# Optimization experiments

Hardware: AMD Instinct MI355X
Metric: run time of the kernel (lower is better)

Reference implementation:

```python
import jax, jax.numpy as jnp
import numpy as np

N, E, D, L, G = 10000, 320000, 256, 5, 128
RWSE, DEG_V = 16, 1001
BN_EPS = 1e-5


def setup_inputs() -> dict:
    key = jax.random.key(0)
    ks = jax.random.split(key, 12)
    s = 1.0 / np.sqrt(D)
    return {
        'feat_id': jax.random.randint(ks[0], (N,), 0, 100000, dtype=jnp.int64 if jax.config.jax_enable_x64 else jnp.int32),
        'edge_index': jax.random.randint(ks[1], (2, E), 0, N),
        'batch_idx': jnp.sort(jax.random.randint(ks[2], (N,), 0, G)),
        'rwse': jax.random.normal(ks[3], (N, RWSE), jnp.float32),
        'in_degrees': jax.random.randint(ks[4], (N,), 0, DEG_V),
        # value_projection: Linear(fixed_input_dim=D -> D); stored as [in, out]
        'w_val': jax.random.normal(ks[5], (D, D), jnp.float32) * s,
        'b_val': jnp.zeros((D,), jnp.float32),
        # rwse_projection: Linear(RWSE -> D)
        'w_rwse': jax.random.normal(ks[6], (RWSE, D), jnp.float32) * (1.0 / np.sqrt(RWSE)),
        'b_rwse': jnp.zeros((D,), jnp.float32),
        # degree_embedding table (clamped to [0, 1000])
        'deg_emb': jax.random.normal(ks[7], (DEG_V, D), jnp.float32) * 0.02,
        # per-layer GIN MLP: Linear-ReLU-Linear, stacked over L layers
        'mlp_w1': jax.random.normal(ks[8], (L, D, D), jnp.float32) * s,
        'mlp_b1': jnp.zeros((L, D), jnp.float32),
        'mlp_w2': jax.random.normal(ks[9], (L, D, D), jnp.float32) * s,
        'mlp_b2': jnp.zeros((L, D), jnp.float32),
        # BatchNorm1d (eval mode: running stats)
        'bn_gamma': jnp.ones((L, D), jnp.float32),
        'bn_beta': jnp.zeros((L, D), jnp.float32),
        'bn_mean': jnp.zeros((L, D), jnp.float32),
        'bn_var': jax.random.uniform(ks[10], (L, D), jnp.float32, 0.5, 1.5),
        # GIN eps per layer
        'eps_gin': jnp.zeros((L,), jnp.float32),
    }


def reference(feat_id, edge_index, batch_idx, rwse, in_degrees,
              w_val, b_val, w_rwse, b_rwse, deg_emb,
              mlp_w1, mlp_b1, mlp_w2, mlp_b2,
              bn_gamma, bn_beta, bn_mean, bn_var, eps_gin):
    # --- node feature embedding ---
    h_id = jnp.remainder(feat_id, D)
    h_one = jax.nn.one_hot(h_id, D, dtype=jnp.float32)            # [N, D]
    h = h_one @ w_val + b_val + rwse @ w_rwse + b_rwse            # value + rwse projections
    deg = jnp.clip(in_degrees, 0, 1000)
    h = h + deg_emb[deg]                                          # degree embedding

    src, dst = edge_index[0], edge_index[1]
    for l in range(L):
        # GIN message passing: sum neighbor features into dst (gather -> scatter-add)
        agg = jax.ops.segment_sum(h[src], dst, num_segments=N)    # [N, D]
        y = agg + (1.0 + eps_gin[l]) * h
        # MLP (Linear-ReLU-Linear)
        y = jax.nn.relu(y @ mlp_w1[l] + mlp_b1[l]) @ mlp_w2[l] + mlp_b2[l]
        # BatchNorm1d (eval: running stats) + ReLU
        y = (y - bn_mean[l]) * (bn_gamma[l] * jax.lax.rsqrt(bn_var[l] + BN_EPS)) + bn_beta[l]
        h = jax.nn.relu(y)

    # --- mean pooling per graph ---
    sums = jax.ops.segment_sum(h, batch_idx, num_segments=G)                     # [G, D]
    cnt = jax.ops.segment_sum(jnp.ones((N, 1), h.dtype), batch_idx, num_segments=G)
    graph_feature = sums / jnp.maximum(cnt, 1.0)
    return graph_feature, h
```

## Files before the change

kernel.cpp:

```cpp
#include <hip/hip_runtime.h>
#include <hip/hip_bf16.h>

#define N_NODES 10000
#define N_EDGES 320000
#define DIM     256
#define N_LAYERS 5
#define N_GRAPHS 128
#define RWSE_K  16
#define GBM 16

typedef __bf16 bf16_t;
typedef bf16_t bf16x8 __attribute__((ext_vector_type(8)));
typedef float  f32x4  __attribute__((ext_vector_type(4)));

__device__ inline ushort f2bf(float f) {
    union { float f; unsigned u; } v; v.f = f;
    unsigned r = v.u + 0x7fff + ((v.u >> 16) & 1);
    return (ushort)(r >> 16);
}
__device__ inline float bfbits2f(unsigned hi16) {
    union { unsigned u; float f; } v; v.u = hi16;
    return v.f;
}

__global__ __launch_bounds__(256)
void setup_kernel(const int* __restrict__ feat_id,
                  const float* __restrict__ rwse,
                  const int* __restrict__ in_deg,
                  const float* __restrict__ w_val,
                  const float* __restrict__ b_val,
                  const float* __restrict__ w_rwse,
                  const float* __restrict__ b_rwse,
                  const float* __restrict__ deg_emb,
                  ushort* __restrict__ hb,
                  const int* __restrict__ ei, int* __restrict__ cnt_arr,
                  const float* __restrict__ w1, const float* __restrict__ w2,
                  ushort* __restrict__ wt1, ushort* __restrict__ wt2,
                  const float* __restrict__ gamma, const float* __restrict__ beta,
                  const float* __restrict__ mean, const float* __restrict__ var,
                  const float* __restrict__ b2, float* __restrict__ scale,
                  float* __restrict__ shift) {
    __shared__ float r[RWSE_K];
    __shared__ float t[32][33];
    int b = blockIdx.x;
    int tid = threadIdx.x;
    if (b < N_NODES) {
        int i = b, d = tid;
        if (d < RWSE_K) r[d] = rwse[i * RWSE_K + d];
        __syncthreads();
        int hid = feat_id[i] & (DIM - 1);
        int dg = in_deg[i];
        dg = dg < 0 ? 0 : (dg > 1000 ? 1000 : dg);
        float v = w_val[hid * DIM + d] + b_val[d] + b_rwse[d] + deg_emb[dg * DIM + d];
#pragma unroll
        for (int k = 0; k < RWSE_K; ++k) v += r[k] * w_rwse[k * DIM + d];
        hb[i * DIM + d] = f2bf(v);
    } else if (b < 11250) {
        int e = (b - N_NODES) * 256 + tid;
        if (e < N_EDGES) atomicAdd(&cnt_arr[ei[N_EDGES + e]], 1);
    } else if (b < 11890) {
        int w_id = b - 11250;
        int l = w_id >> 7;
        int rem = w_id & 127;
        int mat = rem >> 6;
        int tile = rem & 63;
        const float* W  = (mat ? w2  : w1)  + (size_t)l * DIM * DIM;
        ushort*      Wt = (mat ? wt2 : wt1) + (size_t)l * DIM * DIM;
        int k0 = (tile >> 3) * 32, n0 = (tile & 7) * 32;
        int tx = tid & 31, ty = tid >> 5;
#pragma unroll
        for (int j = 0; j < 4; ++j)
            t[ty + j * 8][tx] = W[(k0 + ty + j * 8) * DIM + n0 + tx];
        __syncthreads();
#pragma unroll
        for (int j = 0; j < 4; ++j)
            Wt[(n0 + ty + j * 8) * DIM + k0 + tx] = f2bf(t[tx][ty + j * 8]);
    } else {
        int l = b - 11890;
        int idx = l * DIM + tid;
        float s = gamma[idx] * rsqrtf(var[idx] + 1e-5f);
        scale[idx] = s;
        shift[idx] = beta[idx] + (b2[idx] - mean[idx]) * s;
    }
}

__global__ __launch_bounds__(1024)
void scan_kernel(const int* __restrict__ cnt_arr, int* __restrict__ cur, int n) {
    __shared__ int wsum[16];
    __shared__ int carry_sh;
    int tid = threadIdx.x, wave = tid >> 6, lane = tid & 63;
    if (tid == 0) carry_sh = 0;
    __syncthreads();
    for (int base = 0; base < n; base += 1024) {
        int idx = base + tid;
        int v = (idx < n) ? cnt_arr[idx] : 0;
        int s = v;
#pragma unroll
        for (int off = 1; off < 64; off <<= 1) {
            int t = __shfl_up(s, off, 64);
            if (lane >= off) s += t;
        }
        if (lane == 63) wsum[wave] = s;
        __syncthreads();
        if (wave == 0) {
            int ws = (lane < 16) ? wsum[lane] : 0;
#pragma unroll
            for (int off = 1; off < 16; off <<= 1) {
                int t = __shfl_up(ws, off, 64);
                if (lane >= off) ws += t;
            }
            if (lane < 16) wsum[lane] = ws;
        }
        __syncthreads();
        int excl = s - v + (wave ? wsum[wave - 1] : 0) + carry_sh;
        if (idx < n) cur[idx] = excl;
        __syncthreads();
        if (tid == 0) carry_sh += wsum[15];
        __syncthreads();
    }
}

__global__ __launch_bounds__(256)
void fill_kernel(const int* __restrict__ ei, int* __restrict__ cur,
                 int* __restrict__ cs) {
    int e = blockIdx.x * 256 + threadIdx.x;
    if (e < N_EDGES) {
        int d = ei[N_EDGES + e];
        int p = atomicAdd(&cur[d], 1);
        cs[p] = ei[e];
    }
}

#define ACCV(v)                                                        \
    acc[0] += bfbits2f((v).x << 16); acc[1] += bfbits2f((v).x & 0xffff0000u); \
    acc[2] += bfbits2f((v).y << 16); acc[3] += bfbits2f((v).y & 0xffff0000u); \
    acc[4] += bfbits2f((v).z << 16); acc[5] += bfbits2f((v).z & 0xffff0000u); \
    acc[6] += bfbits2f((v).w << 16); acc[7] += bfbits2f((v).w & 0xffff0000u);

__global__ __launch_bounds__(256)
void agg_kernel(const ushort* __restrict__ hb,
                const int* __restrict__ cur, const int* __restrict__ cs,
                const float* __restrict__ eps_gin, int layer,
                ushort* __restrict__ y) {
    int wave = threadIdx.x >> 6;
    int lane = threadIdx.x & 63;
    int half = lane >> 5;
    int sl   = lane & 31;
    int i = blockIdx.x * 4 + wave;
    if (i >= N_NODES) return;
    const uint4* hb4 = (const uint4*)hb;
    float acc[8];
#pragma unroll
    for (int t = 0; t < 8; ++t) acc[t] = 0.f;

    int e0 = i ? cur[i - 1] : 0;
    int e1 = cur[i];
    for (int base = e0; base < e1; base += 64) {
        int rem = e1 - base;
        int cnt = rem < 64 ? rem : 64;
        int idx = (base + lane < e1) ? cs[base + lane] : 0;
        int j = 0;
        for (; j + 8 <= cnt; j += 8) {
            int s0 = __shfl(idx, j + half, 64);
            int s1 = __shfl(idx, j + 2 + half, 64);
            int s2 = __shfl(idx, j + 4 + half, 64);
            int s3 = __shfl(idx, j + 6 + half, 64);
            uint4 v0 = hb4[(size_t)s0 * 32 + sl];
            uint4 v1 = hb4[(size_t)s1 * 32 + sl];
            uint4 v2 = hb4[(size_t)s2 * 32 + sl];
            uint4 v3 = hb4[(size_t)s3 * 32 + sl];
            ACCV(v0); ACCV(v1); ACCV(v2); ACCV(v3);
        }
        for (; j + 2 <= cnt; j += 2) {
            int s = __shfl(idx, j + half, 64);
            uint4 v = hb4[(size_t)s * 32 + sl];
            ACCV(v);
        }
        if (j < cnt) {
            int s = __shfl(idx, j, 64);
            if (half == 0) {
                uint4 v = hb4[(size_t)s * 32 + sl];
                ACCV(v);
            }
        }
    }
#pragma unroll
    for (int t = 0; t < 8; ++t) acc[t] += __shfl_xor(acc[t], 32, 64);
    if (half == 0) {
        float sc = 1.0f + eps_gin[layer];
        uint4 sv = hb4[(size_t)i * 32 + sl];
        acc[0] += bfbits2f(sv.x << 16) * sc; acc[1] += bfbits2f(sv.x & 0xffff0000u) * sc;
        acc[2] += bfbits2f(sv.y << 16) * sc; acc[3] += bfbits2f(sv.y & 0xffff0000u) * sc;
        acc[4] += bfbits2f(sv.z << 16) * sc; acc[5] += bfbits2f(sv.z & 0xffff0000u) * sc;
        acc[6] += bfbits2f(sv.w << 16) * sc; acc[7] += bfbits2f(sv.w & 0xffff0000u) * sc;
        uint4 o;
        o.x = (uint)f2bf(acc[0]) | ((uint)f2bf(acc[1]) << 16);
        o.y = (uint)f2bf(acc[2]) | ((uint)f2bf(acc[3]) << 16);
        o.z = (uint)f2bf(acc[4]) | ((uint)f2bf(acc[5]) << 16);
        o.w = (uint)f2bf(acc[6]) | ((uint)f2bf(acc[7]) << 16);
        ((uint4*)y)[(size_t)i * 32 + sl] = o;
    }
}

__global__ __launch_bounds__(256)
void gemm12_kernel(const ushort* __restrict__ A, const ushort* __restrict__ Wt1,
                   const float* __restrict__ b1, const ushort* __restrict__ Wt2,
                   const float* __restrict__ bnsc, const float* __restrict__ bnsh,
                   float* __restrict__ outF, ushort* __restrict__ outB, int nrows) {
    __shared__ __align__(16) ushort As[GBM][40];
    __shared__ __align__(16) ushort Bs[DIM][40];
    __shared__ __align__(16) ushort Ts[GBM][DIM + 8];
    int tx = threadIdx.x;
    int row0 = blockIdx.x * GBM;
    int wave = tx >> 6, lane = tx & 63, quad = lane >> 4, l16 = lane & 15;
    int wc = wave * 64;
    int srow = tx >> 2;
    int skol = (tx & 3) * 8;

    f32x4 acc[4];
#pragma unroll
    for (int t = 0; t < 4; ++t) acc[t] = (f32x4){0.f, 0.f, 0.f, 0.f};

    for (int k0 = 0; k0 < DIM; k0 += 32) {
        if (tx < 64) {
            int arow = row0 + srow;
            uint4 av = make_uint4(0u, 0u, 0u, 0u);
            if (arow < nrows) av = *(const uint4*)&A[(size_t)arow * DIM + k0 + skol];
            *(uint4*)&As[srow][skol] = av;
        }
#pragma unroll
        for (int j = 0; j < 4; ++j) {
            int r = srow + 64 * j;
            *(uint4*)&Bs[r][skol] = *(const uint4*)&Wt1[(size_t)r * DIM + k0 + skol];
        }
        __syncthreads();
        bf16x8 af = *(const bf16x8*)&As[l16][quad * 8];
#pragma unroll
        for (int tj = 0; tj < 4; ++tj) {
            bf16x8 bf = *(const bf16x8*)&Bs[wc + tj * 16 + l16][quad * 8];
            acc[tj] = __builtin_amdgcn_mfma_f32_16x16x32_bf16(af, bf, acc[tj], 0, 0, 0);
        }
        __syncthreads();
    }
#pragma unroll
    for (int tj = 0; tj < 4; ++tj) {
        int col = wc + tj * 16 + l16;
        float bias = b1[col];
#pragma unroll
        for (int r = 0; r < 4; ++r)
            Ts[quad * 4 + r][col] = f2bf(fmaxf(acc[tj][r] + bias, 0.f));
    }
    __syncthreads();

#pragma unroll
    for (int t = 0; t < 4; ++t) acc[t] = (f32x4){0.f, 0.f, 0.f, 0.f};
    for (int k0 = 0; k0 < DIM; k0 += 32) {
#pragma unroll
        for (int j = 0; j < 4; ++j) {
            int r = srow + 64 * j;
            *(uint4*)&Bs[r][skol] = *(const uint4*)&Wt2[(size_t)r * DIM + k0 + skol];
        }
        __syncthreads();
        bf16x8 af = *(const bf16x8*)&Ts[l16][k0 + quad * 8];
#pragma unroll
        for (int tj = 0; tj < 4; ++tj) {
            bf16x8 bf = *(const bf16x8*)&Bs[wc + tj * 16 + l16][quad * 8];
            acc[tj] = __builtin_amdgcn_mfma_f32_16x16x32_bf16(af, bf, acc[tj], 0, 0, 0);
        }
        __syncthreads();
    }
#pragma unroll
    for (int tj = 0; tj < 4; ++tj) {
        int col = wc + tj * 16 + l16;
        float s = bnsc[col], sh = bnsh[col];
#pragma unroll
        for (int r = 0; r < 4; ++r) {
            int row = row0 + quad * 4 + r;
            if (row < nrows) {
                float v = fmaxf(acc[tj][r] * s + sh, 0.f);
                if (outF) outF[(size_t)row * DIM + col] = v;
                if (outB) outB[(size_t)row * DIM + col] = f2bf(v);
            }
        }
    }
}

__global__ __launch_bounds__(256)
void pool_kernel(const float* __restrict__ hfin, const int* __restrict__ batch,
                 float* __restrict__ out) {
    int g = blockIdx.x;
    int d = threadIdx.x;
    int l = 0, r = N_NODES;
    while (l < r) { int m = (l + r) >> 1; if (batch[m] < g) l = m + 1; else r = m; }
    int lo = l;
    r = N_NODES;
    while (l < r) { int m = (l + r) >> 1; if (batch[m] < g + 1) l = m + 1; else r = m; }
    int hi = l;
    float a0 = 0.f, a1 = 0.f, a2 = 0.f, a3 = 0.f;
    int i = lo;
    for (; i + 4 <= hi; i += 4) {
        a0 += hfin[(size_t)i * DIM + d];
        a1 += hfin[(size_t)(i + 1) * DIM + d];
        a2 += hfin[(size_t)(i + 2) * DIM + d];
        a3 += hfin[(size_t)(i + 3) * DIM + d];
    }
    for (; i < hi; ++i) a0 += hfin[(size_t)i * DIM + d];
    float c = (float)(hi - lo);
    if (c < 1.f) c = 1.f;
    out[g * DIM + d] = ((a0 + a1) + (a2 + a3)) / c;
}

extern "C" void kernel_launch(void* const* d_in, const int* in_sizes, int n_in,
                              void* d_out, int out_size, void* d_ws, size_t ws_size,
                              hipStream_t stream) {
    const int*   feat_id  = (const int*)d_in[0];
    const int*   ei       = (const int*)d_in[1];
    const int*   batch    = (const int*)d_in[2];
    const float* rwse     = (const float*)d_in[3];
    const int*   in_deg   = (const int*)d_in[4];
    const float* w_val    = (const float*)d_in[5];
    const float* b_val    = (const float*)d_in[6];
    const float* w_rwse   = (const float*)d_in[7];
    const float* b_rwse   = (const float*)d_in[8];
    const float* deg_emb  = (const float*)d_in[9];
    const float* mlp_w1   = (const float*)d_in[10];
    const float* mlp_b1   = (const float*)d_in[11];
    const float* mlp_w2   = (const float*)d_in[12];
    const float* mlp_b2   = (const float*)d_in[13];
    const float* bn_gamma = (const float*)d_in[14];
    const float* bn_beta  = (const float*)d_in[15];
    const float* bn_mean  = (const float*)d_in[16];
    const float* bn_var   = (const float*)d_in[17];
    const float* eps_gin  = (const float*)d_in[18];

    float* out = (float*)d_out;
    float* out_h = out + N_GRAPHS * DIM;

    char* w = (char*)d_ws;
    ushort* hb   = (ushort*)w;
    ushort* y    = hb + (size_t)N_NODES * DIM;
    ushort* wt1  = y + (size_t)N_NODES * DIM;
    ushort* wt2  = wt1 + (size_t)N_LAYERS * DIM * DIM;
    int* cnt_arr = (int*)(wt2 + (size_t)N_LAYERS * DIM * DIM);
    int* cur     = cnt_arr + N_NODES;
    int* cs      = cur + N_NODES;
    float* bnsc  = (float*)(cs + N_EDGES);
    float* bnsh  = bnsc + N_LAYERS * DIM;

    hipMemsetAsync(cnt_arr, 0, N_NODES * sizeof(int), stream);

    setup_kernel<<<11895, 256, 0, stream>>>(
        feat_id, rwse, in_deg, w_val, b_val, w_rwse, b_rwse, deg_emb,
        hb, ei, cnt_arr, mlp_w1, mlp_w2, wt1, wt2,
        bn_gamma, bn_beta, bn_mean, bn_var, mlp_b2, bnsc, bnsh);
    scan_kernel<<<1, 1024, 0, stream>>>(cnt_arr, cur, N_NODES);
    fill_kernel<<<(N_EDGES + 255) / 256, 256, 0, stream>>>(ei, cur, cs);

    int agrid = (N_NODES + 3) / 4;
    int ggrid = (N_NODES + GBM - 1) / GBM;
    for (int l = 0; l < N_LAYERS; ++l) {
        agg_kernel<<<agrid, 256, 0, stream>>>(hb, cur, cs, eps_gin, l, y);
        bool last = (l == N_LAYERS - 1);
        gemm12_kernel<<<ggrid, 256, 0, stream>>>(
            y, wt1 + (size_t)l * DIM * DIM, mlp_b1 + l * DIM,
            wt2 + (size_t)l * DIM * DIM, bnsc + l * DIM, bnsh + l * DIM,
            last ? out_h : nullptr, last ? nullptr : hb, N_NODES);
    }

    pool_kernel<<<N_GRAPHS, 256, 0, stream>>>(out_h, batch, out);
}
```

Before: 342.7 us.

## Load weight fragments directly from global memory in fused MLP GEMM, dropping LDS staging

The fused two-layer MLP kernel no longer stages weight tiles through shared memory each k-step. MFMA B-fragments are now read straight from global (L2-cached) weight arrays, and the whole 16-row A tile is loaded into LDS once, then reused as the intermediate buffer. This removes per-iteration barriers and LDS store/load traffic, and the k-loops are partially unrolled so more loads can be in flight. The cost is that every block re-reads both weight matrices from L2 with less-coalesced 16-byte accesses per lane, so performance depends on cache bandwidth and latency hiding.

After: 389.7 us. 1.14x slower.

```diff
diff --git a/kernel.cpp b/kernel.cpp
--- a/kernel.cpp
+++ b/kernel.cpp
@@ -207,68 +207,64 @@
                    const float* __restrict__ b1, const ushort* __restrict__ Wt2,
                    const float* __restrict__ bnsc, const float* __restrict__ bnsh,
                    float* __restrict__ outF, ushort* __restrict__ outB, int nrows) {
-    __shared__ __align__(16) ushort As[GBM][40];
-    __shared__ __align__(16) ushort Bs[DIM][40];
-    __shared__ __align__(16) ushort Ts[GBM][DIM + 8];
+    __shared__ __align__(16) ushort AT[GBM][DIM + 8];
     int tx = threadIdx.x;
     int row0 = blockIdx.x * GBM;
     int wave = tx >> 6, lane = tx & 63, quad = lane >> 4, l16 = lane & 15;
     int wc = wave * 64;
-    int srow = tx >> 2;
-    int skol = (tx & 3) * 8;
+
+    {
+        int r = tx >> 4;
+        int c = (tx & 15) * 16;
+        int arow = row0 + r;
+        uint4 av0 = make_uint4(0u, 0u, 0u, 0u);
+        uint4 av1 = make_uint4(0u, 0u, 0u, 0u);
+        if (arow < nrows) {
+            av0 = *(const uint4*)&A[(size_t)arow * DIM + c];
+            av1 = *(const uint4*)&A[(size_t)arow * DIM + c + 8];
+        }
+        *(uint4*)&AT[r][c] = av0;
+        *(uint4*)&AT[r][c + 8] = av1;
+    }
+    __syncthreads();
 
     f32x4 acc[4];
 #pragma unroll
     for (int t = 0; t < 4; ++t) acc[t] = (f32x4){0.f, 0.f, 0.f, 0.f};
 
+#pragma unroll 4
     for (int k0 = 0; k0 < DIM; k0 += 32) {
-        if (tx < 64) {
-            int arow = row0 + srow;
-            uint4 av = make_uint4(0u, 0u, 0u, 0u);
-            if (arow < nrows) av = *(const uint4*)&A[(size_t)arow * DIM + k0 + skol];
-            *(uint4*)&As[srow][skol] = av;
-        }
-#pragma unroll
-        for (int j = 0; j < 4; ++j) {
-            int r = srow + 64 * j;
-            *(uint4*)&Bs[r][skol] = *(const uint4*)&Wt1[(size_t)r * DIM + k0 + skol];
-        }
-        __syncthreads();
-        bf16x8 af = *(const bf16x8*)&As[l16][quad * 8];
+        bf16x8 af = *(const bf16x8*)&AT[l16][k0 + quad * 8];
 #pragma unroll
         for (int tj = 0; tj < 4; ++tj) {
-            bf16x8 bf = *(const bf16x8*)&Bs[wc + tj * 16 + l16][quad * 8];
+            bf16x8 bf = *(const bf16x8*)&Wt1[(size_t)(wc + tj * 16 + l16) * DIM + k0 + quad * 8];
             acc[tj] = __builtin_amdgcn_mfma_f32_16x16x32_bf16(af, bf, acc[tj], 0, 0, 0);
         }
-        __syncthreads();
-    }
+    }
+    __syncthreads();
+
 #pragma unroll
     for (int tj = 0; tj < 4; ++tj) {
         int col = wc + tj * 16 + l16;
         float bias = b1[col];
 #pragma unroll
         for (int r = 0; r < 4; ++r)
-            Ts[quad * 4 + r][col] = f2bf(fmaxf(acc[tj][r] + bias, 0.f));
+            AT[quad * 4 + r][col] = f2bf(fmaxf(acc[tj][r] + bias, 0.f));
     }
     __syncthreads();
 
 #pragma unroll
     for (int t = 0; t < 4; ++t) acc[t] = (f32x4){0.f, 0.f, 0.f, 0.f};
+#pragma unroll 4
     for (int k0 = 0; k0 < DIM; k0 += 32) {
-#pragma unroll
-        for (int j = 0; j < 4; ++j) {
-            int r = srow + 64 * j;
-            *(uint4*)&Bs[r][skol] = *(const uint4*)&Wt2[(size_t)r * DIM + k0 + skol];
-        }
-        __syncthreads();
-        bf16x8 af = *(const bf16x8*)&Ts[l16][k0 + quad * 8];
+        bf16x8 af = *(const bf16x8*)&AT[l16][k0 + quad * 8];
 #pragma unroll
         for (int tj = 0; tj < 4; ++tj) {
-            bf16x8 bf = *(const bf16x8*)&Bs[wc + tj * 16 + l16][quad * 8];
+            bf16x8 bf = *(const bf16x8*)&Wt2[(size_t)(wc + tj * 16 + l16) * DIM + k0 + quad * 8];
             acc[tj] = __builtin_amdgcn_mfma_f32_16x16x32_bf16(af, bf, acc[tj], 0, 0, 0);
         }
-        __syncthreads();
-    }
+    }
+
 #pragma unroll
     for (int tj = 0; tj < 4; ++tj) {
         int col = wc + tj * 16 + l16;
```

## Fuse per-layer aggregation, MLP and pooling into one cooperative persistent kernel

Applied to the files above, without the earlier changes.

Replaces the ten per-layer aggregation and GEMM launches plus the pooling launch with a single cooperative kernel. It loops over layers with grid-stride work and uses grid-wide barriers between the aggregation and MLP phases. The goal is to remove kernel launch overhead and inter-kernel gaps. The cost is that grid.sync barriers and a capped, occupancy-bounded grid size may leave load imbalance. A fallback to the original multi-kernel path is kept for when the cooperative launch fails.

Measured after the change: 1.202 ms. 3.51x slower.

```diff
diff --git a/kernel.cpp b/kernel.cpp
--- a/kernel.cpp
+++ b/kernel.cpp
@@ -1,5 +1,8 @@
 #include <hip/hip_runtime.h>
 #include <hip/hip_bf16.h>
+#include <hip/hip_cooperative_groups.h>
+
+namespace cg = cooperative_groups;
 
 #define N_NODES 10000
 #define N_EDGES 320000
@@ -8,6 +11,7 @@
 #define N_GRAPHS 128
 #define RWSE_K  16
 #define GBM 16
+#define NCHUNKS ((N_NODES + GBM - 1) / GBM)
 
 typedef __bf16 bf16_t;
 typedef bf16_t bf16x8 __attribute__((ext_vector_type(8)));
@@ -137,22 +141,14 @@
     acc[4] += bfbits2f((v).z << 16); acc[5] += bfbits2f((v).z & 0xffff0000u); \
     acc[6] += bfbits2f((v).w << 16); acc[7] += bfbits2f((v).w & 0xffff0000u);
 
-__global__ __launch_bounds__(256)
-void agg_kernel(const ushort* __restrict__ hb,
-                const int* __restrict__ cur, const int* __restrict__ cs,
-                const float* __restrict__ eps_gin, int layer,
-                ushort* __restrict__ y) {
-    int wave = threadIdx.x >> 6;
-    int lane = threadIdx.x & 63;
-    int half = lane >> 5;
-    int sl   = lane & 31;
-    int i = blockIdx.x * 4 + wave;
-    if (i >= N_NODES) return;
-    const uint4* hb4 = (const uint4*)hb;
+__device__ __forceinline__ void agg_node(int i, int lane, int half, int sl,
+                                         const uint4* hb4,
+                                         const int* __restrict__ cur,
+                                         const int* __restrict__ cs,
+                                         float sc, ushort* __restrict__ y) {
     float acc[8];
 #pragma unroll
     for (int t = 0; t < 8; ++t) acc[t] = 0.f;
-
     int e0 = i ? cur[i - 1] : 0;
     int e1 = cur[i];
     for (int base = e0; base < e1; base += 64) {
@@ -187,7 +183,6 @@
 #pragma unroll
     for (int t = 0; t < 8; ++t) acc[t] += __shfl_xor(acc[t], 32, 64);
     if (half == 0) {
-        float sc = 1.0f + eps_gin[layer];
         uint4 sv = hb4[(size_t)i * 32 + sl];
         acc[0] += bfbits2f(sv.x << 16) * sc; acc[1] += bfbits2f(sv.x & 0xffff0000u) * sc;
         acc[2] += bfbits2f(sv.y << 16) * sc; acc[3] += bfbits2f(sv.y & 0xffff0000u) * sc;
@@ -202,30 +197,21 @@
     }
 }
 
-__global__ __launch_bounds__(256)
-void gemm12_kernel(const ushort* __restrict__ A, const ushort* __restrict__ Wt1,
-                   const float* __restrict__ b1, const ushort* __restrict__ Wt2,
-                   const float* __restrict__ bnsc, const float* __restrict__ bnsh,
-                   float* __restrict__ outF, ushort* __restrict__ outB, int nrows) {
-    __shared__ __align__(16) ushort As[GBM][40];
-    __shared__ __align__(16) ushort Bs[DIM][40];
-    __shared__ __align__(16) ushort Ts[GBM][DIM + 8];
-    int tx = threadIdx.x;
-    int row0 = blockIdx.x * GBM;
-    int wave = tx >> 6, lane = tx & 63, quad = lane >> 4, l16 = lane & 15;
-    int wc = wave * 64;
-    int srow = tx >> 2;
-    int skol = (tx & 3) * 8;
-
+__device__ __forceinline__ void mlp_chunk(
+        int row0, int tx, int wave, int quad, int l16, int srow, int skol, int wc,
+        ushort (*As)[40], ushort (*Bs)[40], ushort (*Ts)[DIM + 8],
+        const ushort* __restrict__ Ain, const ushort* __restrict__ Wt1,
+        const float* __restrict__ b1, const ushort* __restrict__ Wt2,
+        const float* __restrict__ bnsc, const float* __restrict__ bnsh,
+        float* __restrict__ outF, ushort* __restrict__ outB) {
     f32x4 acc[4];
 #pragma unroll
     for (int t = 0; t < 4; ++t) acc[t] = (f32x4){0.f, 0.f, 0.f, 0.f};
-
     for (int k0 = 0; k0 < DIM; k0 += 32) {
         if (tx < 64) {
             int arow = row0 + srow;
             uint4 av = make_uint4(0u, 0u, 0u, 0u);
-            if (arow < nrows) av = *(const uint4*)&A[(size_t)arow * DIM + k0 + skol];
+            if (arow < N_NODES) av = *(const uint4*)&Ain[(size_t)arow * DIM + k0 + skol];
             *(uint4*)&As[srow][skol] = av;
         }
 #pragma unroll
@@ -251,7 +237,6 @@
             Ts[quad * 4 + r][col] = f2bf(fmaxf(acc[tj][r] + bias, 0.f));
     }
     __syncthreads();
-
 #pragma unroll
     for (int t = 0; t < 4; ++t) acc[t] = (f32x4){0.f, 0.f, 0.f, 0.f};
     for (int k0 = 0; k0 < DIM; k0 += 32) {
@@ -276,7 +261,7 @@
 #pragma unroll
         for (int r = 0; r < 4; ++r) {
             int row = row0 + quad * 4 + r;
-            if (row < nrows) {
+            if (row < N_NODES) {
                 float v = fmaxf(acc[tj][r] * s + sh, 0.f);
                 if (outF) outF[(size_t)row * DIM + col] = v;
                 if (outB) outB[(size_t)row * DIM + col] = f2bf(v);
@@ -285,11 +270,9 @@
     }
 }
 
-__global__ __launch_bounds__(256)
-void pool_kernel(const float* __restrict__ hfin, const int* __restrict__ batch,
-                 float* __restrict__ out) {
-    int g = blockIdx.x;
-    int d = threadIdx.x;
+__device__ __forceinline__ void pool_graph(int g, int d, const float* __restrict__ out_h,
+                                           const int* __restrict__ batch,
+                                           float* __restrict__ out) {
     int l = 0, r = N_NODES;
     while (l < r) { int m = (l + r) >> 1; if (batch[m] < g) l = m + 1; else r = m; }
     int lo = l;
@@ -299,15 +282,93 @@
     float a0 = 0.f, a1 = 0.f, a2 = 0.f, a3 = 0.f;
     int i = lo;
     for (; i + 4 <= hi; i += 4) {
-        a0 += hfin[(size_t)i * DIM + d];
-        a1 += hfin[(size_t)(i + 1) * DIM + d];
-        a2 += hfin[(size_t)(i + 2) * DIM + d];
-        a3 += hfin[(size_t)(i + 3) * DIM + d];
-    }
-    for (; i < hi; ++i) a0 += hfin[(size_t)i * DIM + d];
+        a0 += out_h[(size_t)i * DIM + d];
+        a1 += out_h[(size_t)(i + 1) * DIM + d];
+        a2 += out_h[(size_t)(i + 2) * DIM + d];
+        a3 += out_h[(size_t)(i + 3) * DIM + d];
+    }
+    for (; i < hi; ++i) a0 += out_h[(size_t)i * DIM + d];
     float c = (float)(hi - lo);
     if (c < 1.f) c = 1.f;
     out[g * DIM + d] = ((a0 + a1) + (a2 + a3)) / c;
+}
+
+__global__ __launch_bounds__(256, 4)
+void net_kernel(ushort* __restrict__ hb, ushort* __restrict__ y,
+                const int* __restrict__ cur, const int* __restrict__ cs,
+                const float* __restrict__ eps_gin,
+                const ushort* __restrict__ wt1, const ushort* __restrict__ wt2,
+                const float* __restrict__ b1all,
+                const float* __restrict__ bnscAll, const float* __restrict__ bnshAll,
+                const int* __restrict__ batch, float* __restrict__ out) {
+    cg::grid_group grid = cg::this_grid();
+    __shared__ __align__(16) ushort As[GBM][40];
+    __shared__ __align__(16) ushort Bs[DIM][40];
+    __shared__ __align__(16) ushort Ts[GBM][DIM + 8];
+    float* out_h = out + N_GRAPHS * DIM;
+
+    int tx = threadIdx.x;
+    int wave = tx >> 6, lane = tx & 63, half = lane >> 5, sl = lane & 31;
+    int quad = lane >> 4, l16 = lane & 15;
+    int gwave = blockIdx.x * 4 + wave;
+    const int nwaves = gridDim.x * 4;
+    int srow = tx >> 2;
+    int skol = (tx & 3) * 8;
+    int wc = wave * 64;
+
+    for (int l = 0; l < N_LAYERS; ++l) {
+        float sc = 1.0f + eps_gin[l];
+        const uint4* hb4 = (const uint4*)hb;
+        for (int i = gwave; i < N_NODES; i += nwaves)
+            agg_node(i, lane, half, sl, hb4, cur, cs, sc, y);
+        grid.sync();
+
+        const ushort* Wt1 = wt1 + (size_t)l * DIM * DIM;
+        const ushort* Wt2 = wt2 + (size_t)l * DIM * DIM;
+        bool last = (l == N_LAYERS - 1);
+        for (int c = blockIdx.x; c < NCHUNKS; c += gridDim.x)
+            mlp_chunk(c * GBM, tx, wave, quad, l16, srow, skol, wc, As, Bs, Ts,
+                      y, Wt1, b1all + l * DIM, Wt2,
+                      bnscAll + l * DIM, bnshAll + l * DIM,
+                      last ? out_h : nullptr, last ? nullptr : hb);
+        grid.sync();
+    }
+
+    if (blockIdx.x < N_GRAPHS)
+        pool_graph(blockIdx.x, tx, out_h, batch, out);
+}
+
+__global__ __launch_bounds__(256)
+void agg_kernel(const ushort* __restrict__ hb,
+                const int* __restrict__ cur, const int* __restrict__ cs,
+                const float* __restrict__ eps_gin, int layer,
+                ushort* __restrict__ y) {
+    int wave = threadIdx.x >> 6;
+    int lane = threadIdx.x & 63;
+    int i = blockIdx.x * 4 + wave;
+    if (i >= N_NODES) return;
+    agg_node(i, lane, lane >> 5, lane & 31, (const uint4*)hb, cur, cs,
+             1.0f + eps_gin[layer], y);
+}
+
+__global__ __launch_bounds__(256)
+void gemm12_kernel(const ushort* __restrict__ A, const ushort* __restrict__ Wt1,
+                   const float* __restrict__ b1, const ushort* __restrict__ Wt2,
+                   const float* __restrict__ bnsc, const float* __restrict__ bnsh,
+                   float* __restrict__ outF, ushort* __restrict__ outB) {
+    __shared__ __align__(16) ushort As[GBM][40];
+    __shared__ __align__(16) ushort Bs[DIM][40];
+    __shared__ __align__(16) ushort Ts[GBM][DIM + 8];
+    int tx = threadIdx.x;
+    int wave = tx >> 6, lane = tx & 63, quad = lane >> 4, l16 = lane & 15;
+    mlp_chunk(blockIdx.x * GBM, tx, wave, quad, l16, tx >> 2, (tx & 3) * 8,
+              wave * 64, As, Bs, Ts, A, Wt1, b1, Wt2, bnsc, bnsh, outF, outB);
+}
+
+__global__ __launch_bounds__(256)
+void pool_kernel(const float* __restrict__ hfin, const int* __restrict__ batch,
+                 float* __restrict__ out) {
+    pool_graph(blockIdx.x, threadIdx.x, hfin, batch, out);
 }
 
 extern "C" void kernel_launch(void* const* d_in, const int* in_sizes, int n_in,
@@ -356,16 +417,35 @@
     scan_kernel<<<1, 1024, 0, stream>>>(cnt_arr, cur, N_NODES);
     fill_kernel<<<(N_EDGES + 255) / 256, 256, 0, stream>>>(ei, cur, cs);
 
-    int agrid = (N_NODES + 3) / 4;
-    int ggrid = (N_NODES + GBM - 1) / GBM;
-    for (int l = 0; l < N_LAYERS; ++l) {
-        agg_kernel<<<agrid, 256, 0, stream>>>(hb, cur, cs, eps_gin, l, y);
-        bool last = (l == N_LAYERS - 1);
-        gemm12_kernel<<<ggrid, 256, 0, stream>>>(
-            y, wt1 + (size_t)l * DIM * DIM, mlp_b1 + l * DIM,
-            wt2 + (size_t)l * DIM * DIM, bnsc + l * DIM, bnsh + l * DIM,
-            last ? out_h : nullptr, last ? nullptr : hb, N_NODES);
-    }
-
-    pool_kernel<<<N_GRAPHS, 256, 0, stream>>>(out_h, batch, out);
-}
+    int perCU = 0;
+    hipError_t qerr = hipOccupancyMaxActiveBlocksPerMultiprocessor(
+        &perCU, (const void*)net_kernel, 256, 0);
+    bool coop_ok = (qerr == hipSuccess && perCU >= 1);
+    if (coop_ok) {
+        int grid = perCU * 256;
+        if (grid > 1024) grid = 1024;
+        if (grid < N_GRAPHS) coop_ok = false;
+        if (coop_ok) {
+            void* kargs[] = {
+                (void*)&hb, (void*)&y, (void*)&cur, (void*)&cs, (void*)&eps_gin,
+                (void*)&wt1, (void*)&wt2, (void*)&mlp_b1, (void*)&bnsc, (void*)&bnsh,
+                (void*)&batch, (void*)&out
+            };
+            hipError_t lerr = hipLaunchCooperativeKernel(
+                (const void*)net_kernel, dim3(grid), dim3(256), kargs, 0, stream);
+            if (lerr != hipSuccess) coop_ok = false;
+        }
+    }
+    if (!coop_ok) {
+        int agrid = (N_NODES + 3) / 4;
+        for (int l = 0; l < N_LAYERS; ++l) {
+            agg_kernel<<<agrid, 256, 0, stream>>>(hb, cur, cs, eps_gin, l, y);
+            bool last = (l == N_LAYERS - 1);
+            gemm12_kernel<<<NCHUNKS, 256, 0, stream>>>(
+                y, wt1 + (size_t)l * DIM * DIM, mlp_b1 + l * DIM,
+                wt2 + (size_t)l * DIM * DIM, bnsc + l * DIM, bnsh + l * DIM,
+                last ? out_h : nullptr, last ? nullptr : hb);
+        }
+        pool_kernel<<<N_GRAPHS, 256, 0, stream>>>(out_h, batch, out);
+    }
+}
```
